# Kernel tuning notes

Hardware: AMD Instinct MI355X
Metric: run time of the kernel (lower is better)

## Reference

```python
import jax, jax.numpy as jnp
import numpy as np

EPS = 1e-4

def softmax_kernel(data, projection, is_query):
    # data: [b,h,s,d], projection: [m,d] -> phi(data): [b,h,s,m]
    d = data.shape[-1]
    m = projection.shape[0]
    data_normalizer = d ** -0.25
    ratio = m ** -0.5
    # projected logits
    data_dash = jnp.einsum('bhsd,md->bhsm', data_normalizer * data, projection)
    # ||x||^2 / 2 * normalizer^2, per token
    diag_data = 0.5 * (data_normalizer ** 2) * jnp.sum(data * data, axis=-1, keepdims=True)
    if is_query:
        stab = jnp.max(data_dash, axis=-1, keepdims=True)          # per-token max
    else:
        stab = jnp.max(data_dash, axis=(-2, -1), keepdims=True)    # per (b,h) max
    return ratio * (jnp.exp(data_dash - diag_data - stab) + EPS)

def setup_inputs() -> dict:
    key = jax.random.key(0)
    kq, kk, kp = jax.random.split(key, 3)
    b, h, s, d, m = 2, 16, 4096, 64, 256
    q = jax.random.normal(kq, (b, h, s, d), dtype=jnp.float32)
    k = jax.random.normal(kk, (b, h, s, d), dtype=jnp.float32)
    projection_matrix = jax.random.normal(kp, (m, d), dtype=jnp.float32)
    return {"q": q, "k": k, "projection_matrix": projection_matrix}

def reference(q, k, projection_matrix):
    q_prime = softmax_kernel(q, projection_matrix, is_query=True)
    k_prime = softmax_kernel(k, projection_matrix, is_query=False)
    return (q_prime, k_prime)
```

## Files before the change

### kernel.cpp

```cpp
#include <hip/hip_runtime.h>
#include <math.h>

#define D 64
#define M 256
#define NTOK 131072ull
#define QOUT_ELEMS 33554432ull

constexpr float DATA_NORM  = 0.35355339059327373f;
constexpr float DIAG_SCALE = 0.0625f;
constexpr float RATIO      = 0.0625f;
constexpr float EPS_F      = 1e-4f;

__global__ __launch_bounds__(256) void k0_transpose(const float* __restrict__ proj,
                                                    float* __restrict__ projT) {
    int i = blockIdx.x * 256 + threadIdx.x;
    int m = i >> 6, d = i & 63;
    projT[d * M + m] = proj[i];
}

__global__ __launch_bounds__(256, 2) void k1_main(
    const float* __restrict__ qin, const float* __restrict__ kin,
    const float* __restrict__ projT, float* __restrict__ out,
    float* __restrict__ partial_max)
{
    __shared__ float proj_lds[D * M];
    __shared__ float x_lds[4][16][D];

    const int tid  = threadIdx.x;
    const int lane = tid & 63;
    const int wave = tid >> 6;
    const int bid  = blockIdx.x;
    const bool is_q = (bid < 512);
    const float* __restrict__ src = is_q ? qin : kin;
    const int tb = is_q ? bid : (bid - 512);
    float* __restrict__ outbase = out + (is_q ? 0ull : QOUT_ELEMS);

    {
        const float4* g = (const float4*)projT;
        float4* l = (float4*)proj_lds;
        #pragma unroll
        for (int i = 0; i < 16; ++i) l[i * 256 + tid] = g[i * 256 + tid];
    }
    __syncthreads();

    float blockmax = -INFINITY;

    for (int pass = 0; pass < 4; ++pass) {
        const int token0 = tb * 256 + pass * 64 + wave * 16;

        const float4* g = (const float4*)(src + (size_t)token0 * D);
        float4* xl = (float4*)(&x_lds[wave][0][0]);
        float4 xv[4];
        #pragma unroll
        for (int kk = 0; kk < 4; ++kk) xv[kk] = g[kk * 64 + lane];
        #pragma unroll
        for (int kk = 0; kk < 4; ++kk) xl[kk * 64 + lane] = xv[kk];

        float dsum[4];
        #pragma unroll
        for (int kk = 0; kk < 4; ++kk)
            dsum[kk] = xv[kk].x*xv[kk].x + xv[kk].y*xv[kk].y
                     + xv[kk].z*xv[kk].z + xv[kk].w*xv[kk].w;
        #pragma unroll
        for (int off = 1; off < 16; off <<= 1) {
            #pragma unroll
            for (int kk = 0; kk < 4; ++kk)
                dsum[kk] += __shfl_xor(dsum[kk], off);
        }
        float diag[16];
        #pragma unroll
        for (int tt = 0; tt < 16; ++tt)
            diag[tt] = __shfl(dsum[tt >> 2], (tt & 3) * 16) * DIAG_SCALE;

        __syncthreads();

        float4 acc[16];
        #pragma unroll
        for (int tt = 0; tt < 16; ++tt) acc[tt] = make_float4(0.f, 0.f, 0.f, 0.f);

        for (int d4 = 0; d4 < 16; ++d4) {
            float4 pv[4];
            #pragma unroll
            for (int i = 0; i < 4; ++i)
                pv[i] = *(const float4*)&proj_lds[(4 * d4 + i) * M + 4 * lane];
            #pragma unroll
            for (int tt = 0; tt < 16; ++tt) {
                float4 xq = *(const float4*)&x_lds[wave][tt][4 * d4];
                acc[tt].x = fmaf(pv[0].x, xq.x, acc[tt].x);
                acc[tt].y = fmaf(pv[0].y, xq.x, acc[tt].y);
                acc[tt].z = fmaf(pv[0].z, xq.x, acc[tt].z);
                acc[tt].w = fmaf(pv[0].w, xq.x, acc[tt].w);
                acc[tt].x = fmaf(pv[1].x, xq.y, acc[tt].x);
                acc[tt].y = fmaf(pv[1].y, xq.y, acc[tt].y);
                acc[tt].z = fmaf(pv[1].z, xq.y, acc[tt].z);
                acc[tt].w = fmaf(pv[1].w, xq.y, acc[tt].w);
                acc[tt].x = fmaf(pv[2].x, xq.z, acc[tt].x);
                acc[tt].y = fmaf(pv[2].y, xq.z, acc[tt].y);
                acc[tt].z = fmaf(pv[2].z, xq.z, acc[tt].z);
                acc[tt].w = fmaf(pv[2].w, xq.z, acc[tt].w);
                acc[tt].x = fmaf(pv[3].x, xq.w, acc[tt].x);
                acc[tt].y = fmaf(pv[3].y, xq.w, acc[tt].y);
                acc[tt].z = fmaf(pv[3].z, xq.w, acc[tt].z);
                acc[tt].w = fmaf(pv[3].w, xq.w, acc[tt].w);
            }
        }

        if (is_q) {
            #pragma unroll
            for (int tt = 0; tt < 16; ++tt) {
                float4 dd;
                dd.x = acc[tt].x * DATA_NORM;
                dd.y = acc[tt].y * DATA_NORM;
                dd.z = acc[tt].z * DATA_NORM;
                dd.w = acc[tt].w * DATA_NORM;
                float mx = fmaxf(fmaxf(dd.x, dd.y), fmaxf(dd.z, dd.w));
                #pragma unroll
                for (int off = 1; off < 64; off <<= 1)
                    mx = fmaxf(mx, __shfl_xor(mx, off));
                const float c = diag[tt] + mx;
                float4 o;
                o.x = RATIO * (expf(dd.x - c) + EPS_F);
                o.y = RATIO * (expf(dd.y - c) + EPS_F);
                o.z = RATIO * (expf(dd.z - c) + EPS_F);
                o.w = RATIO * (expf(dd.w - c) + EPS_F);
                ((float4*)outbase)[(size_t)(token0 + tt) * 64 + lane] = o;
            }
        } else {
            #pragma unroll
            for (int tt = 0; tt < 16; ++tt) {
                float4 dd;
                dd.x = acc[tt].x * DATA_NORM;
                dd.y = acc[tt].y * DATA_NORM;
                dd.z = acc[tt].z * DATA_NORM;
                dd.w = acc[tt].w * DATA_NORM;
                blockmax = fmaxf(blockmax, fmaxf(fmaxf(dd.x, dd.y), fmaxf(dd.z, dd.w)));
                float4 o;
                o.x = dd.x - diag[tt];
                o.y = dd.y - diag[tt];
                o.z = dd.z - diag[tt];
                o.w = dd.w - diag[tt];
                ((float4*)outbase)[(size_t)(token0 + tt) * 64 + lane] = o;
            }
        }
        __syncthreads();
    }

    if (!is_q) {
        #pragma unroll
        for (int off = 1; off < 64; off <<= 1)
            blockmax = fmaxf(blockmax, __shfl_xor(blockmax, off));
        if (lane == 0) x_lds[0][0][wave] = blockmax;
        __syncthreads();
        if (tid == 0) {
            float m0 = fmaxf(fmaxf(x_lds[0][0][0], x_lds[0][0][1]),
                             fmaxf(x_lds[0][0][2], x_lds[0][0][3]));
            partial_max[bid - 512] = m0;
        }
    }
}

__global__ void k2_reduce(const float* __restrict__ partial, float* __restrict__ stab) {
    int tid = threadIdx.x;
    float v = partial[tid];
    #pragma unroll
    for (int off = 1; off < 16; off <<= 1)
        v = fmaxf(v, __shfl_xor(v, off));
    if ((tid & 15) == 0) stab[tid >> 4] = v;
}

__global__ __launch_bounds__(256) void k3_fix(float* __restrict__ outk,
                                              const float* __restrict__ stab) {
    const int bid = blockIdx.x;
    const float st = stab[bid >> 6];
    float4* p = (float4*)outk + (size_t)bid * 4096;
    const int tid = threadIdx.x;
    #pragma unroll 4
    for (int it = 0; it < 16; ++it) {
        float4 v = p[it * 256 + tid];
        float4 o;
        o.x = RATIO * (expf(v.x - st) + EPS_F);
        o.y = RATIO * (expf(v.y - st) + EPS_F);
        o.z = RATIO * (expf(v.z - st) + EPS_F);
        o.w = RATIO * (expf(v.w - st) + EPS_F);
        p[it * 256 + tid] = o;
    }
}

extern "C" void kernel_launch(void* const* d_in, const int* in_sizes, int n_in,
                              void* d_out, int out_size, void* d_ws, size_t ws_size,
                              hipStream_t stream) {
    const float* q    = (const float*)d_in[0];
    const float* k    = (const float*)d_in[1];
    const float* proj = (const float*)d_in[2];
    float* out = (float*)d_out;
    float* ws  = (float*)d_ws;

    float* projT   = ws;
    float* partial = ws + 16384;
    float* stab    = ws + 16384 + 512;

    k0_transpose<<<64,   256, 0, stream>>>(proj, projT);
    k1_main     <<<1024, 256, 0, stream>>>(q, k, projT, out, partial);
    k2_reduce   <<<1,    512, 0, stream>>>(partial, stab);
    k3_fix      <<<2048, 256, 0, stream>>>(out + QOUT_ELEMS, stab);
}
```

Measured before the change: 428.1 us.

## Use 512-thread blocks, fold log2e into exp2, merge reduce into fix

Doubles the block to 8 waves, each handling 8 tokens per pass instead of 16. This halves the accumulator register footprint and allows more resident waves. It also folds log2(e) into the scale constants so the exponentials become exp2f, and removes the separate single-block max-reduce kernel by having each fix block reduce its own 16 partials. The trade-off is more LDS reads of the projection per FMA, because each wave now reuses a projection load across fewer tokens.

```diff
diff --git a/kernel.cpp b/kernel.cpp
--- a/kernel.cpp
+++ b/kernel.cpp
@@ -3,13 +3,14 @@
 
 #define D 64
 #define M 256
-#define NTOK 131072ull
 #define QOUT_ELEMS 33554432ull
 
-constexpr float DATA_NORM  = 0.35355339059327373f;
-constexpr float DIAG_SCALE = 0.0625f;
-constexpr float RATIO      = 0.0625f;
-constexpr float EPS_F      = 1e-4f;
+constexpr float DATA_NORM = 0.35355339059327373f;
+constexpr float L2E       = 1.4426950408889634f;
+constexpr float DN_L2E    = DATA_NORM * L2E;
+constexpr float DIAG_L2E  = 0.0625f * L2E;
+constexpr float RATIO     = 0.0625f;
+constexpr float EPS_F     = 1e-4f;
 
 __global__ __launch_bounds__(256) void k0_transpose(const float* __restrict__ proj,
                                                     float* __restrict__ projT) {
@@ -18,13 +19,13 @@
     projT[d * M + m] = proj[i];
 }
 
-__global__ __launch_bounds__(256, 2) void k1_main(
+__global__ __launch_bounds__(512, 4) void k1_main(
     const float* __restrict__ qin, const float* __restrict__ kin,
     const float* __restrict__ projT, float* __restrict__ out,
     float* __restrict__ partial_max)
 {
     __shared__ float proj_lds[D * M];
-    __shared__ float x_lds[4][16][D];
+    __shared__ float x_lds[8][8][D];
 
     const int tid  = threadIdx.x;
     const int lane = tid & 63;
@@ -39,44 +40,44 @@
         const float4* g = (const float4*)projT;
         float4* l = (float4*)proj_lds;
         #pragma unroll
-        for (int i = 0; i < 16; ++i) l[i * 256 + tid] = g[i * 256 + tid];
+        for (int i = 0; i < 8; ++i) l[i * 512 + tid] = g[i * 512 + tid];
     }
     __syncthreads();
 
     float blockmax = -INFINITY;
 
     for (int pass = 0; pass < 4; ++pass) {
-        const int token0 = tb * 256 + pass * 64 + wave * 16;
+        const int token0 = tb * 256 + pass * 64 + wave * 8;
 
         const float4* g = (const float4*)(src + (size_t)token0 * D);
         float4* xl = (float4*)(&x_lds[wave][0][0]);
-        float4 xv[4];
-        #pragma unroll
-        for (int kk = 0; kk < 4; ++kk) xv[kk] = g[kk * 64 + lane];
-        #pragma unroll
-        for (int kk = 0; kk < 4; ++kk) xl[kk * 64 + lane] = xv[kk];
-
-        float dsum[4];
-        #pragma unroll
-        for (int kk = 0; kk < 4; ++kk)
+        float4 xv[2];
+        #pragma unroll
+        for (int kk = 0; kk < 2; ++kk) xv[kk] = g[kk * 64 + lane];
+        #pragma unroll
+        for (int kk = 0; kk < 2; ++kk) xl[kk * 64 + lane] = xv[kk];
+
+        float dsum[2];
+        #pragma unroll
+        for (int kk = 0; kk < 2; ++kk)
             dsum[kk] = xv[kk].x*xv[kk].x + xv[kk].y*xv[kk].y
                      + xv[kk].z*xv[kk].z + xv[kk].w*xv[kk].w;
         #pragma unroll
         for (int off = 1; off < 16; off <<= 1) {
             #pragma unroll
-            for (int kk = 0; kk < 4; ++kk)
+            for (int kk = 0; kk < 2; ++kk)
                 dsum[kk] += __shfl_xor(dsum[kk], off);
         }
-        float diag[16];
-        #pragma unroll
-        for (int tt = 0; tt < 16; ++tt)
-            diag[tt] = __shfl(dsum[tt >> 2], (tt & 3) * 16) * DIAG_SCALE;
+        float diag[8];
+        #pragma unroll
+        for (int tt = 0; tt < 8; ++tt)
+            diag[tt] = __shfl(dsum[tt >> 2], (tt & 3) * 16) * DIAG_L2E;
 
         __syncthreads();
 
-        float4 acc[16];
-        #pragma unroll
-        for (int tt = 0; tt < 16; ++tt) acc[tt] = make_float4(0.f, 0.f, 0.f, 0.f);
+        float4 acc[8];
+        #pragma unroll
+        for (int tt = 0; tt < 8; ++tt) acc[tt] = make_float4(0.f, 0.f, 0.f, 0.f);
 
         for (int d4 = 0; d4 < 16; ++d4) {
             float4 pv[4];
@@ -84,7 +85,7 @@
             for (int i = 0; i < 4; ++i)
                 pv[i] = *(const float4*)&proj_lds[(4 * d4 + i) * M + 4 * lane];
             #pragma unroll
-            for (int tt = 0; tt < 16; ++tt) {
+            for (int tt = 0; tt < 8; ++tt) {
                 float4 xq = *(const float4*)&x_lds[wave][tt][4 * d4];
                 acc[tt].x = fmaf(pv[0].x, xq.x, acc[tt].x);
                 acc[tt].y = fmaf(pv[0].y, xq.x, acc[tt].y);
@@ -107,32 +108,32 @@
 
         if (is_q) {
             #pragma unroll
-            for (int tt = 0; tt < 16; ++tt) {
+            for (int tt = 0; tt < 8; ++tt) {
                 float4 dd;
-                dd.x = acc[tt].x * DATA_NORM;
-                dd.y = acc[tt].y * DATA_NORM;
-                dd.z = acc[tt].z * DATA_NORM;
-                dd.w = acc[tt].w * DATA_NORM;
+                dd.x = acc[tt].x * DN_L2E;
+                dd.y = acc[tt].y * DN_L2E;
+                dd.z = acc[tt].z * DN_L2E;
+                dd.w = acc[tt].w * DN_L2E;
                 float mx = fmaxf(fmaxf(dd.x, dd.y), fmaxf(dd.z, dd.w));
                 #pragma unroll
                 for (int off = 1; off < 64; off <<= 1)
                     mx = fmaxf(mx, __shfl_xor(mx, off));
                 const float c = diag[tt] + mx;
                 float4 o;
-                o.x = RATIO * (expf(dd.x - c) + EPS_F);
-                o.y = RATIO * (expf(dd.y - c) + EPS_F);
-                o.z = RATIO * (expf(dd.z - c) + EPS_F);
-                o.w = RATIO * (expf(dd.w - c) + EPS_F);
+                o.x = RATIO * (exp2f(dd.x - c) + EPS_F);
+                o.y = RATIO * (exp2f(dd.y - c) + EPS_F);
+                o.z = RATIO * (exp2f(dd.z - c) + EPS_F);
+                o.w = RATIO * (exp2f(dd.w - c) + EPS_F);
                 ((float4*)outbase)[(size_t)(token0 + tt) * 64 + lane] = o;
             }
         } else {
             #pragma unroll
-            for (int tt = 0; tt < 16; ++tt) {
+            for (int tt = 0; tt < 8; ++tt) {
                 float4 dd;
-                dd.x = acc[tt].x * DATA_NORM;
-                dd.y = acc[tt].y * DATA_NORM;
-                dd.z = acc[tt].z * DATA_NORM;
-                dd.w = acc[tt].w * DATA_NORM;
+                dd.x = acc[tt].x * DN_L2E;
+                dd.y = acc[tt].y * DN_L2E;
+                dd.z = acc[tt].z * DN_L2E;
+                dd.w = acc[tt].w * DN_L2E;
                 blockmax = fmaxf(blockmax, fmaxf(fmaxf(dd.x, dd.y), fmaxf(dd.z, dd.w)));
                 float4 o;
                 o.x = dd.x - diag[tt];
@@ -152,36 +153,34 @@
         if (lane == 0) x_lds[0][0][wave] = blockmax;
         __syncthreads();
         if (tid == 0) {
-            float m0 = fmaxf(fmaxf(x_lds[0][0][0], x_lds[0][0][1]),
-                             fmaxf(x_lds[0][0][2], x_lds[0][0][3]));
-            partial_max[bid - 512] = m0;
-        }
-    }
-}
-
-__global__ void k2_reduce(const float* __restrict__ partial, float* __restrict__ stab) {
-    int tid = threadIdx.x;
-    float v = partial[tid];
+            float m0 = -INFINITY;
+            #pragma unroll
+            for (int w = 0; w < 8; ++w) m0 = fmaxf(m0, x_lds[0][0][w]);
+            partial_max[tb] = m0;
+        }
+    }
+}
+
+__global__ __launch_bounds__(256) void k3_fix(float* __restrict__ outk,
+                                              const float* __restrict__ partial) {
+    const int bid = blockIdx.x;
+    const int bh  = bid >> 6;
+    const int tid = threadIdx.x;
+    float v = partial[bh * 16 + (tid & 15)];
     #pragma unroll
     for (int off = 1; off < 16; off <<= 1)
         v = fmaxf(v, __shfl_xor(v, off));
-    if ((tid & 15) == 0) stab[tid >> 4] = v;
-}
-
-__global__ __launch_bounds__(256) void k3_fix(float* __restrict__ outk,
-                                              const float* __restrict__ stab) {
-    const int bid = blockIdx.x;
-    const float st = stab[bid >> 6];
+    const float st = v;
+
     float4* p = (float4*)outk + (size_t)bid * 4096;
-    const int tid = threadIdx.x;
     #pragma unroll 4
     for (int it = 0; it < 16; ++it) {
-        float4 v = p[it * 256 + tid];
+        float4 w = p[it * 256 + tid];
         float4 o;
-        o.x = RATIO * (expf(v.x - st) + EPS_F);
-        o.y = RATIO * (expf(v.y - st) + EPS_F);
-        o.z = RATIO * (expf(v.z - st) + EPS_F);
-        o.w = RATIO * (expf(v.w - st) + EPS_F);
+        o.x = RATIO * (exp2f(w.x - st) + EPS_F);
+        o.y = RATIO * (exp2f(w.y - st) + EPS_F);
+        o.z = RATIO * (exp2f(w.z - st) + EPS_F);
+        o.w = RATIO * (exp2f(w.w - st) + EPS_F);
         p[it * 256 + tid] = o;
     }
 }
@@ -197,10 +196,8 @@
 
     float* projT   = ws;
     float* partial = ws + 16384;
-    float* stab    = ws + 16384 + 512;
 
     k0_transpose<<<64,   256, 0, stream>>>(proj, projT);
-    k1_main     <<<1024, 256, 0, stream>>>(q, k, projT, out, partial);
-    k2_reduce   <<<1,    512, 0, stream>>>(partial, stab);
-    k3_fix      <<<2048, 256, 0, stream>>>(out + QOUT_ELEMS, stab);
-}
+    k1_main     <<<1024, 512, 0, stream>>>(q, k, projT, out, partial);
+    k3_fix      <<<2048, 256, 0, stream>>>(out + QOUT_ELEMS, partial);
+}
```

Measured after the change: 423.9 us. About the same (-1.0%).
